# Optimization experiments

Measured on AMD Instinct MI355X. Metric: run time of the kernel, lower is better.

Reference implementation:

```python
import jax, jax.numpy as jnp
import numpy as np

N = 100000   # num_nodes
R = 200      # num_relations
DIM = 200    # hidden dim (in = out for every layer)
B = 30       # num_bases
L = 2        # num_layers
E = 800000   # num_edges


def setup_inputs() -> dict:
    key = jax.random.key(0)
    ks = jax.random.split(key, 7)
    edge_index = jax.random.randint(ks[0], (2, E), 0, N)
    edge_type = jax.random.randint(ks[1], (E,), 0, R)
    s = 1.0 / np.sqrt(DIM)
    emb = jax.random.normal(ks[2], (N, DIM), jnp.float32)
    comp = jax.random.normal(ks[3], (L, R, B), jnp.float32) * (1.0 / np.sqrt(B))
    bases = jax.random.normal(ks[4], (L, B, DIM, DIM), jnp.float32) * s
    root = jax.random.normal(ks[5], (L, DIM, DIM), jnp.float32) * s
    bias = jnp.zeros((L, DIM), jnp.float32)
    return dict(edge_index=edge_index, edge_type=edge_type, emb=emb,
                comp=comp, bases=bases, root=root, bias=bias)


def _rgcn_layer(x, src, dst, etype, comp_l, bases_l, root_l, bias_l):
    # Basis decomposition: W_r = sum_b comp[r, b] * bases[b]
    # msg_e = x[src_e] @ W_{etype_e}  computed as sum over bases (B is small & fixed)
    x_src = x[src]                      # [E, DIM] gather
    c = comp_l[etype]                   # [E, B] per-edge basis coefficients

    def body(acc, bc):
        basis_b, c_b = bc               # [DIM, DIM], [E]
        return acc + c_b[:, None] * (x_src @ basis_b), None

    acc0 = jnp.zeros((x_src.shape[0], root_l.shape[1]), x.dtype)
    msg, _ = jax.lax.scan(body, acc0, (bases_l, jnp.swapaxes(c, 0, 1)))  # [E, DIM]

    # PyG RGCNConv mean aggregation: normalize by in-degree per (dst node, relation)
    comb = dst * R + etype
    deg = jax.ops.segment_sum(jnp.ones((etype.shape[0],), x.dtype), comb,
                              num_segments=N * R)
    norm = 1.0 / jnp.maximum(deg[comb], 1.0)                             # [E]

    agg = jax.ops.segment_sum(msg * norm[:, None], dst, num_segments=N)  # [N, DIM]
    return agg + x @ root_l + bias_l


def reference(edge_index, edge_type, emb, comp, bases, root, bias):
    src, dst = edge_index[0], edge_index[1]
    x = emb
    for l in range(L):
        x = jax.nn.relu(_rgcn_layer(x, src, dst, edge_type,
                                    comp[l], bases[l], root[l], bias[l]))
        # dropout is identity in eval mode (deterministic reference)
    return x
```

## Files before the change

### kernel.cpp

```cpp
#include <hip/hip_runtime.h>
#include <hip/hip_bf16.h>
#include <stdint.h>

#define NN 100000
#define RR 200
#define DD 200
#define BB 30
#define LL 2
#define EE 800000

#define KP 224
#define NP 208
#define XP 224
#define AP 232
#define BPL 200
#define RT 128
#define MSGP 200
#define NSPL 2
#define MAXNC 24
#define NPART 128
#define EPB ((EE + NPART - 1) / NPART)

using bf16x8 = __attribute__((ext_vector_type(8))) short;
using f32x4  = __attribute__((ext_vector_type(4))) float;

#define OFF_NORM   0ull
#define OFF_SORT   3200000ull
#define OFF_CNT    6400000ull
#define OFF_XB     6404096ull
#define OFF_WT     51204096ull
#define OFF_ROOTT  69840896ull
#define OFF_CTL    69934080ull
#define OFF_POS    70065152ull
#define OFF_DSTCNT 73265152ull
#define OFF_DSTST  73665152ull
#define OFF_CUR    74065184ull
#define OFF_BLKH   74465184ull

static __device__ __forceinline__ short f2bf(float v) {
    union { __hip_bfloat16 h; short s; } u;
    u.h = __float2bfloat16(v);
    return u.s;
}

__global__ void kCount(const int* __restrict__ ei, const int* __restrict__ et,
                       unsigned int* __restrict__ deg8, int* __restrict__ dstCnt, int big) {
    int e = blockIdx.x * 256 + threadIdx.x;
    if (e >= EE) return;
    int d = ei[EE + e];
    int t = et[e];
    int comb = d * RR + t;
    atomicAdd(&deg8[comb >> 2], 1u << ((comb & 3) * 8));
    if (big) atomicAdd(&dstCnt[d], 1);
}

__global__ void kScanBlk(const int* __restrict__ dstCnt, int* __restrict__ dstStart,
                         int* __restrict__ blkSum) {
    __shared__ int s[256];
    int t = threadIdx.x, i = blockIdx.x * 256 + t;
    int v = (i < NN) ? dstCnt[i] : 0;
    s[t] = v;
    __syncthreads();
    #pragma unroll
    for (int off = 1; off < 256; off <<= 1) {
        int x = (t >= off) ? s[t - off] : 0;
        __syncthreads();
        s[t] += x;
        __syncthreads();
    }
    if (i < NN) dstStart[i] = s[t] - v;
    if (t == 255) blkSum[blockIdx.x] = s[255];
}
__global__ void kScanTop(int* __restrict__ blkSum, int nblk) {
    __shared__ int s[512];
    int t = threadIdx.x;
    int v = (t < nblk) ? blkSum[t] : 0;
    s[t] = v;
    __syncthreads();
    #pragma unroll
    for (int off = 1; off < 512; off <<= 1) {
        int x = (t >= off) ? s[t - off] : 0;
        __syncthreads();
        s[t] += x;
        __syncthreads();
    }
    if (t < nblk) blkSum[t] = s[t] - v;
}
__global__ void kScanAdd(const int* __restrict__ dstCnt, int* __restrict__ dstStart,
                         const int* __restrict__ blkSum) {
    int i = blockIdx.x * 256 + threadIdx.x;
    if (i >= NN) return;
    int v = dstStart[i] + blkSum[blockIdx.x];
    dstStart[i] = v;
    if (i == NN - 1) dstStart[NN] = v + dstCnt[i];
}

__global__ void kChunk(const int* __restrict__ dstStart, int* __restrict__ bS,
                       int* __restrict__ cesS, int NC, int T) {
    int tid = threadIdx.x;
    if (tid > NC) return;
    int v;
    if (tid == NC) v = NN;
    else if (tid == 0) v = 0;
    else {
        int target = tid * T;
        int lo = 0, hi = NN;
        while (lo < hi) {
            int mid = (lo + hi) >> 1;
            if (dstStart[mid] >= target) hi = mid; else lo = mid + 1;
        }
        v = lo;
    }
    bS[tid] = v;
    cesS[tid] = dstStart[v];
}

__global__ __launch_bounds__(256) void kHist(const int* __restrict__ ei,
        const int* __restrict__ et, const int* __restrict__ bS,
        int* __restrict__ blockHist, int NC) {
    __shared__ int hist[MAXNC * RR];
    __shared__ int bsh[MAXNC + 1];
    int tid = threadIdx.x, b = blockIdx.x;
    int NB = NC * RR;
    if (tid <= NC) bsh[tid] = bS[tid];
    for (int i = tid; i < NB; i += 256) hist[i] = 0;
    __syncthreads();
    int ebeg = b * EPB, eend = min(EE, ebeg + EPB);
    for (int e = ebeg + tid; e < eend; e += 256) {
        int d = ei[EE + e];
        int t = et[e];
        int c = 0;
        for (int j = 1; j < NC; ++j) if (d >= bsh[j]) c = j;
        atomicAdd(&hist[c * RR + t], 1);
    }
    __syncthreads();
    for (int i = tid; i < NB; i += 256)
        blockHist[(size_t)b * NB + i] = hist[i];
}

__global__ __launch_bounds__(128) void kScanP(int* __restrict__ blockHist,
                                              int* __restrict__ cntB, int NB) {
    __shared__ int s[NPART];
    int t = threadIdx.x, k = blockIdx.x;
    int v = blockHist[(size_t)t * NB + k];
    s[t] = v;
    __syncthreads();
    #pragma unroll
    for (int off = 1; off < NPART; off <<= 1) {
        int x = (t >= off) ? s[t - off] : 0;
        __syncthreads();
        s[t] += x;
        __syncthreads();
    }
    blockHist[(size_t)t * NB + k] = s[t] - v;
    if (t == NPART - 1) cntB[k] = s[NPART - 1];
}

__global__ void kScanB(const int* __restrict__ cntB, int* __restrict__ relStartB,
                       int* __restrict__ cursorB, int nb) {
    __shared__ int c[MAXNC * RR];
    __shared__ int rs[MAXNC * RR + 1];
    int tid = threadIdx.x;
    for (int i = tid; i < nb; i += 256) c[i] = cntB[i];
    __syncthreads();
    if (tid == 0) {
        int s = 0;
        for (int i = 0; i < nb; ++i) {
            rs[i] = s;
            s += c[i];
        }
        rs[nb] = s;
    }
    __syncthreads();
    for (int i = tid; i <= nb; i += 256) {
        relStartB[i] = rs[i];
        if (i < nb) cursorB[i] = rs[i];
    }
}

__global__ __launch_bounds__(256) void kPart(const int* __restrict__ ei,
        const int* __restrict__ et, const unsigned int* __restrict__ deg8,
        const int* __restrict__ bS, const int* __restrict__ relStartB,
        const int* __restrict__ blockHist, const int* __restrict__ dstStart,
        int* __restrict__ cur, float* __restrict__ norm, int* __restrict__ sortedE,
        int* __restrict__ posDst, int NC) {
    __shared__ int curL[MAXNC * RR];
    __shared__ int bsh[MAXNC + 1];
    int tid = threadIdx.x, b = blockIdx.x;
    int NB = NC * RR;
    if (tid <= NC) bsh[tid] = bS[tid];
    for (int i = tid; i < NB; i += 256)
        curL[i] = relStartB[i] + blockHist[(size_t)b * NB + i];
    __syncthreads();
    int ebeg = b * EPB, eend = min(EE, ebeg + EPB);
    for (int e = ebeg + tid; e < eend; e += 256) {
        int d = ei[EE + e];
        int t = et[e];
        int comb = d * RR + t;
        unsigned int deg = (deg8[comb >> 2] >> ((comb & 3) * 8)) & 0xffu;
        norm[e] = 1.0f / (float)(deg ? deg : 1u);
        int c = 0;
        for (int j = 1; j < NC; ++j) if (d >= bsh[j]) c = j;
        int pos = atomicAdd(&curL[c * RR + t], 1);
        sortedE[pos] = e;
        posDst[e] = dstStart[d] + atomicAdd(&cur[d], 1);
    }
}

__global__ void kCountB(const int* __restrict__ ei, const int* __restrict__ et,
                        const int* __restrict__ bS, int* __restrict__ cntB, int NC) {
    __shared__ int bsh[MAXNC + 1];
    if (threadIdx.x <= NC) bsh[threadIdx.x] = bS[threadIdx.x];
    __syncthreads();
    int e = blockIdx.x * 256 + threadIdx.x;
    if (e >= EE) return;
    int d = ei[EE + e];
    int t = et[e];
    int c = 0;
    for (int j = 1; j < NC; ++j) if (d >= bsh[j]) c = j;
    atomicAdd(&cntB[c * RR + t], 1);
}

__global__ void kNormScatter(const int* __restrict__ ei, const int* __restrict__ et,
                             const unsigned int* __restrict__ deg8, const int* __restrict__ bS,
                             int* __restrict__ cursorB, const int* __restrict__ dstStart,
                             int* __restrict__ cur, float* __restrict__ norm,
                             int* __restrict__ sortedE, int* __restrict__ posDst,
                             int NC, int big) {
    __shared__ int bsh[MAXNC + 1];
    if (threadIdx.x <= NC) bsh[threadIdx.x] = bS[threadIdx.x];
    __syncthreads();
    int e = blockIdx.x * 256 + threadIdx.x;
    if (e >= EE) return;
    int d = ei[EE + e];
    int t = et[e];
    int comb = d * RR + t;
    unsigned int deg = (deg8[comb >> 2] >> ((comb & 3) * 8)) & 0xffu;
    norm[e] = 1.0f / (float)(deg ? deg : 1u);
    int c = 0;
    for (int j = 1; j < NC; ++j) if (d >= bsh[j]) c = j;
    int pos = atomicAdd(&cursorB[c * RR + t], 1);
    sortedE[pos] = e;
    if (big) posDst[e] = dstStart[d] + atomicAdd(&cur[d], 1);
}

__global__ void kConvert(const float* __restrict__ x, short* __restrict__ xb, int doRelu) {
    int idx = blockIdx.x * 256 + threadIdx.x;
    if (idx >= NN * XP) return;
    int i = idx / XP, col = idx - i * XP;
    float v = 0.0f;
    if (col < DD) {
        v = x[i * DD + col];
        if (doRelu) v = fmaxf(v, 0.0f);
    }
    xb[idx] = (col < DD) ? f2bf(v) : (short)0;
}

__global__ void kRelu(float* __restrict__ y) {
    int idx = blockIdx.x * 256 + threadIdx.x;
    if (idx < NN * DD) y[idx] = fmaxf(y[idx], 0.0f);
}

__global__ __launch_bounds__(256) void kW(const float* __restrict__ comp,
                                          const float* __restrict__ bases,
                                          short* __restrict__ Wt) {
    int kt = blockIdx.x;
    int ng = blockIdx.y;
    int tid = threadIdx.x;
    int k = kt * 32 + (tid & 31);
    int n = ng * 8 + (tid >> 5);
    bool live = (k < DD) && (n < DD);
    float vb[BB];
    #pragma unroll
    for (int b = 0; b < BB; ++b)
        vb[b] = live ? bases[((size_t)b * DD + k) * DD + n] : 0.0f;
    size_t wo = (size_t)n * KP + k;
    for (int r = 0; r < RR; ++r) {
        float a = 0.0f;
        #pragma unroll
        for (int b = 0; b < BB; ++b) a += comp[r * BB + b] * vb[b];
        Wt[(size_t)r * (NP * KP) + wo] = f2bf(a);
    }
}

__global__ void kRootT(const float* __restrict__ root, short* __restrict__ rootT) {
    int idx = blockIdx.x * 256 + threadIdx.x;
    if (idx >= NP * KP) return;
    int n = idx / KP, k = idx - n * KP;
    rootT[idx] = (n < DD && k < DD) ? f2bf(root[k * DD + n]) : (short)0;
}

template<int F0, int NF>
__device__ __forceinline__ void gemmHalf2(const short* As, const short* bCol,
                                          int arow0, int arow1, int kg,
                                          f32x4* acc0, f32x4* acc1) {
    #pragma unroll
    for (int f = 0; f < NF; ++f) {
        acc0[f] = (f32x4){0.f, 0.f, 0.f, 0.f};
        acc1[f] = (f32x4){0.f, 0.f, 0.f, 0.f};
    }
    bf16x8 bb[2][NF];
    #pragma unroll
    for (int f = 0; f < NF; ++f)
        bb[0][f] = *(const bf16x8*)(bCol + (size_t)(F0 + f) * 16 * KP);
    #pragma unroll
    for (int kc = 0; kc < 7; ++kc) {
        if (kc < 6) {
            #pragma unroll
            for (int f = 0; f < NF; ++f)
                bb[(kc + 1) & 1][f] = *(const bf16x8*)(bCol + (size_t)(F0 + f) * 16 * KP + (kc + 1) * 32);
        }
        bf16x8 a0 = *(const bf16x8*)(&As[arow0 * AP + kc * 32 + kg]);
        bf16x8 a1 = *(const bf16x8*)(&As[arow1 * AP + kc * 32 + kg]);
        #pragma unroll
        for (int f = 0; f < NF; ++f) {
            acc0[f] = __builtin_amdgcn_mfma_f32_16x16x32_bf16(a0, bb[kc & 1][f], acc0[f], 0, 0, 0);
            acc1[f] = __builtin_amdgcn_mfma_f32_16x16x32_bf16(a1, bb[kc & 1][f], acc1[f], 0, 0, 0);
        }
    }
}

__global__ __launch_bounds__(256) void kRootGemm(const short* __restrict__ xb,
        const short* __restrict__ rootT, const float* __restrict__ bias,
        float* __restrict__ y) {
    __shared__ short As[RT * AP];
    int i0 = blockIdx.x * RT;
    int tid = threadIdx.x;
    int rowL = tid >> 1, sub = tid & 1;
    int i = i0 + rowL;
    for (int c = sub; c < 28; c += 2) {
        int4 v = make_int4(0, 0, 0, 0);
        if (i < NN) v = *(const int4*)(xb + (size_t)i * XP + c * 8);
        *(int4*)(&As[rowL * AP + c * 8]) = v;
    }
    __syncthreads();
    int lane = tid & 63, wave = tid >> 6;
    int arow0 = wave * 32 + (lane & 15);
    int arow1 = arow0 + 16;
    int kg = (lane >> 4) * 8;
    const short* bCol = rootT + (lane & 15) * KP + kg;
    int colLane = lane & 15;
    int rbase = i0 + wave * 32 + (lane >> 4) * 4;
    {
        f32x4 acc0[7], acc1[7];
        gemmHalf2<0, 7>(As, bCol, arow0, arow1, kg, acc0, acc1);
        #pragma unroll
        for (int f = 0; f < 7; ++f) {
            int col = f * 16 + colLane;
            float bv = bias[col];
            #pragma unroll
            for (int j = 0; j < 4; ++j) {
                int r0 = rbase + j, r1 = rbase + 16 + j;
                if (r0 < NN) y[(size_t)r0 * DD + col] = acc0[f][j] + bv;
                if (r1 < NN) y[(size_t)r1 * DD + col] = acc1[f][j] + bv;
            }
        }
    }
    {
        f32x4 acc0[6], acc1[6];
        gemmHalf2<7, 6>(As, bCol, arow0, arow1, kg, acc0, acc1);
        #pragma unroll
        for (int f = 0; f < 6; ++f) {
            int col = (7 + f) * 16 + colLane;
            if (col < DD) {
                float bv = bias[col];
                #pragma unroll
                for (int j = 0; j < 4; ++j) {
                    int r0 = rbase + j, r1 = rbase + 16 + j;
                    if (r0 < NN) y[(size_t)r0 * DD + col] = acc0[f][j] + bv;
                    if (r1 < NN) y[(size_t)r1 * DD + col] = acc1[f][j] + bv;
                }
            }
        }
    }
}

template<int MODE>
__global__ __launch_bounds__(512) void kMsgP(const int* __restrict__ ei,
        const short* __restrict__ xb, const short* __restrict__ Wt,
        const int* __restrict__ relStartB, const int* __restrict__ sortedE,
        const float* __restrict__ norm, const int* __restrict__ posDst,
        const int* __restrict__ cesS, float* __restrict__ y,
        short* __restrict__ msg, int c) {
    __shared__ short Bp[200 * BPL + 64];
    int r = blockIdx.x / NSPL;
    int h = blockIdx.x - r * NSPL;
    int relStart = relStartB[c * RR + r];
    int eEnd     = relStartB[c * RR + r + 1];
    int nE = eEnd - relStart;
    if (nE <= 0) return;
    int tid = threadIdx.x;
    {
        const short* wp = Wt + (size_t)r * (NP * KP);
        for (int idx = tid; idx < 200 * 25; idx += 512) {
            int n = idx / 25, k8 = idx - n * 25;
            int4 v = *(const int4*)(wp + (size_t)n * KP + k8 * 8);
            *(int4*)(&Bp[n * BPL + k8 * 8]) = v;
        }
    }
    __syncthreads();
    int lane = tid & 63, wave = tid >> 6;
    int colLane = lane & 15;
    int kg = (lane >> 4) * 8;
    int rbase = (lane >> 4) * 4;
    int nwt = (nE + 31) / 32;
    int ces = (MODE == 0) ? cesS[c] : 0;

    bf16x8 aC[2][7], aN[2][7];
    int psC[2][4], psN[2][4];
    float nmC[2][4], nmN[2][4];

    auto loadTile = [&](int wt, bf16x8 (*a)[7], int (*ps)[4], float (*nm)[4]) {
        int eBase = relStart + wt * 32;
        #pragma unroll
        for (int m = 0; m < 2; ++m) {
            int eIdxA = eBase + m * 16 + colLane;
            int eidA = sortedE[min(eIdxA, eEnd - 1)];
            int srcA = ei[eidA];
            const short* aRow = xb + (size_t)srcA * XP;
            #pragma unroll
            for (int kc = 0; kc < 7; ++kc)
                a[m][kc] = *(const bf16x8*)(aRow + kc * 32 + kg);
            #pragma unroll
            for (int j = 0; j < 4; ++j) {
                int eI = eBase + m * 16 + rbase + j;
                bool v = eI < eEnd;
                int eid = v ? sortedE[eI] : 0;
                nm[m][j] = v ? norm[eid] : 0.0f;
                if (MODE == 0) ps[m][j] = v ? (posDst[eid] - ces) : -1;
                else           ps[m][j] = v ? ei[EE + eid] : -1;
            }
        }
    };

    int wt = h * 8 + wave;
    if (wt < nwt) loadTile(wt, aC, psC, nmC);
    for (; wt < nwt; wt += NSPL * 8) {
        int wtn = wt + NSPL * 8;
        if (wtn < nwt) loadTile(wtn, aN, psN, nmN);
        {
            f32x4 acc0[7], acc1[7];
            #pragma unroll
            for (int f = 0; f < 7; ++f) {
                acc0[f] = (f32x4){0.f, 0.f, 0.f, 0.f};
                acc1[f] = (f32x4){0.f, 0.f, 0.f, 0.f};
            }
            #pragma unroll
            for (int kc = 0; kc < 7; ++kc) {
                bf16x8 bb[7];
                #pragma unroll
                for (int f = 0; f < 7; ++f)
                    bb[f] = *(const bf16x8*)(&Bp[(f * 16 + colLane) * BPL + kc * 32 + kg]);
                #pragma unroll
                for (int f = 0; f < 7; ++f) {
                    acc0[f] = __builtin_amdgcn_mfma_f32_16x16x32_bf16(aC[0][kc], bb[f], acc0[f], 0, 0, 0);
                    acc1[f] = __builtin_amdgcn_mfma_f32_16x16x32_bf16(aC[1][kc], bb[f], acc1[f], 0, 0, 0);
                }
            }
            #pragma unroll
            for (int m = 0; m < 2; ++m) {
                #pragma unroll
                for (int j = 0; j < 4; ++j) {
                    int ps = psC[m][j]; float nm = nmC[m][j];
                    if (ps >= 0) {
                        #pragma unroll
                        for (int f = 0; f < 7; ++f) {
                            int col = f * 16 + colLane;
                            float val = (m ? acc1[f][j] : acc0[f][j]) * nm;
                            if (MODE == 0) msg[(size_t)ps * MSGP + col] = f2bf(val);
                            else           atomicAdd(&y[(size_t)ps * DD + col], val);
                        }
                    }
                }
            }
        }
        {
            f32x4 acc0[6], acc1[6];
            #pragma unroll
            for (int f = 0; f < 6; ++f) {
                acc0[f] = (f32x4){0.f, 0.f, 0.f, 0.f};
                acc1[f] = (f32x4){0.f, 0.f, 0.f, 0.f};
            }
            #pragma unroll
            for (int kc = 0; kc < 7; ++kc) {
                bf16x8 bb[6];
                #pragma unroll
                for (int f = 0; f < 6; ++f) {
                    int row = (7 + f) * 16 + colLane;
                    row = min(row, 199);
                    bb[f] = *(const bf16x8*)(&Bp[row * BPL + kc * 32 + kg]);
                }
                #pragma unroll
                for (int f = 0; f < 6; ++f) {
                    acc0[f] = __builtin_amdgcn_mfma_f32_16x16x32_bf16(aC[0][kc], bb[f], acc0[f], 0, 0, 0);
                    acc1[f] = __builtin_amdgcn_mfma_f32_16x16x32_bf16(aC[1][kc], bb[f], acc1[f], 0, 0, 0);
                }
            }
            #pragma unroll
            for (int m = 0; m < 2; ++m) {
                #pragma unroll
                for (int j = 0; j < 4; ++j) {
                    int ps = psC[m][j]; float nm = nmC[m][j];
                    if (ps >= 0) {
                        #pragma unroll
                        for (int f = 0; f < 6; ++f) {
                            int col = (7 + f) * 16 + colLane;
                            if (col < DD) {
                                float val = (m ? acc1[f][j] : acc0[f][j]) * nm;
                                if (MODE == 0) msg[(size_t)ps * MSGP + col] = f2bf(val);
                                else           atomicAdd(&y[(size_t)ps * DD + col], val);
                            }
                        }
                    }
                }
            }
        }
        if (wtn < nwt) {
            #pragma unroll
            for (int m = 0; m < 2; ++m) {
                #pragma unroll
                for (int kc = 0; kc < 7; ++kc) aC[m][kc] = aN[m][kc];
                #pragma unroll
                for (int j = 0; j < 4; ++j) { psC[m][j] = psN[m][j]; nmC[m][j] = nmN[m][j]; }
            }
        }
    }
}

__global__ __launch_bounds__(256) void kAgg(const short* __restrict__ msg,
        const int* __restrict__ dstStart, const int* __restrict__ bS,
        const int* __restrict__ cesS, float* __restrict__ y, int c) {
    int wv = threadIdx.x >> 6, lane = threadIdx.x & 63;
    int b0 = bS[c], b1 = bS[c + 1];
    int ces = cesS[c];
    int gw = blockIdx.x * 4 + wv;
    int nw = gridDim.x * 4;
    for (int d = b0 + gw; d < b1; d += nw) {
        int s = dstStart[d] - ces, e = dstStart[d + 1] - ces;
        float a0 = 0.f, a1 = 0.f, a2 = 0.f, a3 = 0.f;
        if (lane < 50) {
            for (int j = s; j < e; ++j) {
                int2 v = *(const int2*)(msg + (size_t)j * MSGP + lane * 4);
                unsigned u0 = (unsigned)v.x, u1 = (unsigned)v.y;
                a0 += __uint_as_float(u0 << 16);
                a1 += __uint_as_float(u0 & 0xffff0000u);
                a2 += __uint_as_float(u1 << 16);
                a3 += __uint_as_float(u1 & 0xffff0000u);
            }
            int colBase = lane * 4;
            float4 rv = *(const float4*)(y + (size_t)d * DD + colBase);
            float4 o;
            o.x = fmaxf(rv.x + a0, 0.f);
            o.y = fmaxf(rv.y + a1, 0.f);
            o.z = fmaxf(rv.z + a2, 0.f);
            o.w = fmaxf(rv.w + a3, 0.f);
            *(float4*)(y + (size_t)d * DD + colBase) = o;
        }
    }
}

extern "C" void kernel_launch(void* const* d_in, const int* in_sizes, int n_in,
                              void* d_out, int out_size, void* d_ws, size_t ws_size,
                              hipStream_t stream) {
    (void)in_sizes; (void)n_in; (void)out_size;
    const int*   ei    = (const int*)d_in[0];
    const int*   et    = (const int*)d_in[1];
    const float* emb   = (const float*)d_in[2];
    const float* comp  = (const float*)d_in[3];
    const float* bases = (const float*)d_in[4];
    const float* root  = (const float*)d_in[5];
    const float* bias  = (const float*)d_in[6];
    float* y = (float*)d_out;
    char* ws = (char*)d_ws;
    float* norm    = (float*)(ws + OFF_NORM);
    int*   sortedE = (int*)(ws + OFF_SORT);
    short* xb      = (short*)(ws + OFF_XB);
    short* Wt      = (short*)(ws + OFF_WT);
    short* rootT   = (short*)(ws + OFF_ROOTT);
    int*   posDst  = (int*)(ws + OFF_POS);
    int*   dstCnt  = (int*)(ws + OFF_DSTCNT);
    int*   dstStart= (int*)(ws + OFF_DSTST);
    int*   cur     = (int*)(ws + OFF_CUR);
    int*   blockHist = (int*)(ws + OFF_BLKH);
    unsigned int* deg8 = (unsigned int*)(ws + OFF_XB);

    int NC = 0;
    long long T = EE;
    unsigned long long msgOff = 0;
    for (int cc = 1; cc <= MAXNC; ++cc) {
        long long t = (EE + cc - 1) / cc;
        unsigned long long mo = OFF_BLKH + (unsigned long long)NPART * cc * RR * 4;
        unsigned long long need = mo + (unsigned long long)(t + 64) * (MSGP * 2);
        if ((unsigned long long)ws_size >= need) { NC = cc; T = t; msgOff = mo; break; }
    }
    int big = (NC > 0) ? 1 : 0;
    if (!big) { NC = 1; T = EE; msgOff = OFF_BLKH; }
    short* msg = (short*)(ws + msgOff);

    int *cntB, *relStartB, *cursorB, *bS, *cesS, *blkSum;
    if (big) {
        int* ctl = (int*)(ws + OFF_CTL);
        cntB = ctl; relStartB = ctl + 4864; cursorB = ctl + 9728;
        bS = ctl + 19456; cesS = ctl + 19520; blkSum = ctl + 19584;
    } else {
        int* ctl = (int*)(ws + OFF_CNT);
        cntB = ctl; relStartB = ctl + 256; cursorB = ctl + 512;
        bS = ctl + 976; cesS = ctl + 992; blkSum = ctl + 1000;
    }

    const int NBLK = (NN + 255) / 256;

    hipMemsetAsync(deg8, 0, (size_t)NN * RR, stream);
    if (big) {
        hipMemsetAsync(dstCnt, 0, (size_t)NN * 4, stream);
        hipMemsetAsync(cur, 0, (size_t)NN * 4, stream);
    } else {
        hipMemsetAsync((void*)cntB, 0, 4096, stream);
    }

    kCount<<<(EE + 255) / 256, 256, 0, stream>>>(ei, et, deg8, dstCnt, big);
    if (big) {
        kScanBlk<<<NBLK, 256, 0, stream>>>(dstCnt, dstStart, blkSum);
        kScanTop<<<1, 512, 0, stream>>>(blkSum, NBLK);
        kScanAdd<<<NBLK, 256, 0, stream>>>(dstCnt, dstStart, blkSum);
        kChunk<<<1, 64, 0, stream>>>(dstStart, bS, cesS, NC, (int)T);
        kHist<<<NPART, 256, 0, stream>>>(ei, et, bS, blockHist, NC);
        kScanP<<<NC * RR, NPART, 0, stream>>>(blockHist, cntB, NC * RR);
        kScanB<<<1, 256, 0, stream>>>(cntB, relStartB, cursorB, NC * RR);
        kPart<<<NPART, 256, 0, stream>>>(ei, et, deg8, bS, relStartB, blockHist,
                                         dstStart, cur, norm, sortedE, posDst, NC);
    } else {
        kCountB<<<(EE + 255) / 256, 256, 0, stream>>>(ei, et, bS, cntB, NC);
        kScanB<<<1, 256, 0, stream>>>(cntB, relStartB, cursorB, NC * RR);
        kNormScatter<<<(EE + 255) / 256, 256, 0, stream>>>(ei, et, deg8, bS, cursorB,
                                                           dstStart, cur, norm, sortedE,
                                                           posDst, NC, big);
    }
    kConvert<<<(NN * XP + 255) / 256, 256, 0, stream>>>(emb, xb, 0);

    for (int l = 0; l < LL; ++l) {
        kW<<<dim3(7, 26), 256, 0, stream>>>(comp + l * RR * BB,
                                            bases + (size_t)l * BB * DD * DD, Wt);
        kRootT<<<(NP * KP + 255) / 256, 256, 0, stream>>>(root + l * DD * DD, rootT);
        kRootGemm<<<(NN + RT - 1) / RT, 256, 0, stream>>>(xb, rootT, bias + l * DD, y);
        if (big) {
            for (int c = 0; c < NC; ++c) {
                kMsgP<0><<<RR * NSPL, 512, 0, stream>>>(ei, xb, Wt, relStartB, sortedE,
                                                        norm, posDst, cesS, y, msg, c);
                kAgg<<<2048, 256, 0, stream>>>(msg, dstStart, bS, cesS, y, c);
            }
            if (l == 0)
                kConvert<<<(NN * XP + 255) / 256, 256, 0, stream>>>(y, xb, 0);
        } else {
            kMsgP<1><<<RR * NSPL, 512, 0, stream>>>(ei, xb, Wt, relStartB, sortedE,
                                                    norm, posDst, cesS, y, msg, 0);
            if (l == 0) kConvert<<<(NN * XP + 255) / 256, 256, 0, stream>>>(y, xb, 1);
            else        kRelu<<<(NN * DD + 255) / 256, 256, 0, stream>>>(y);
        }
    }
}
```

Before: 1.301 ms.

## Shrink LDS weight tile to 160 rows, stream rest from global, drop prefetch

Only the first 160 output rows of each relation's weight matrix are now staged in LDS; the last 48 rows (columns 160-207) are read straight from global memory with a double-buffered register prefetch over k. The register double-buffering of the next edge tile's A fragments and indices is removed. The goal is to cut LDS use and register pressure so more blocks or waves fit per CU. The cost is extra global/L2 weight reads per tile and no overlap of the gather latency with compute.

```diff
diff --git a/kernel.cpp b/kernel.cpp
--- a/kernel.cpp
+++ b/kernel.cpp
@@ -14,6 +14,7 @@
 #define XP 224
 #define AP 232
 #define BPL 200
+#define LROWS 160
 #define RT 128
 #define MSGP 200
 #define NSPL 2
@@ -382,7 +383,7 @@
         const float* __restrict__ norm, const int* __restrict__ posDst,
         const int* __restrict__ cesS, float* __restrict__ y,
         short* __restrict__ msg, int c) {
-    __shared__ short Bp[200 * BPL + 64];
+    __shared__ short Bp[LROWS * BPL + 64];
     int r = blockIdx.x / NSPL;
     int h = blockIdx.x - r * NSPL;
     int relStart = relStartB[c * RR + r];
@@ -390,13 +391,11 @@
     int nE = eEnd - relStart;
     if (nE <= 0) return;
     int tid = threadIdx.x;
-    {
-        const short* wp = Wt + (size_t)r * (NP * KP);
-        for (int idx = tid; idx < 200 * 25; idx += 512) {
-            int n = idx / 25, k8 = idx - n * 25;
-            int4 v = *(const int4*)(wp + (size_t)n * KP + k8 * 8);
-            *(int4*)(&Bp[n * BPL + k8 * 8]) = v;
-        }
+    const short* wp = Wt + (size_t)r * (NP * KP);
+    for (int idx = tid; idx < LROWS * 25; idx += 512) {
+        int n = idx / 25, k8 = idx - n * 25;
+        int4 v = *(const int4*)(wp + (size_t)n * KP + k8 * 8);
+        *(int4*)(&Bp[n * BPL + k8 * 8]) = v;
     }
     __syncthreads();
     int lane = tid & 63, wave = tid >> 6;
@@ -405,12 +404,13 @@
     int rbase = (lane >> 4) * 4;
     int nwt = (nE + 31) / 32;
     int ces = (MODE == 0) ? cesS[c] : 0;
-
-    bf16x8 aC[2][7], aN[2][7];
-    int psC[2][4], psN[2][4];
-    float nmC[2][4], nmN[2][4];
-
-    auto loadTile = [&](int wt, bf16x8 (*a)[7], int (*ps)[4], float (*nm)[4]) {
+    const short* gCol = wp + (size_t)(LROWS + colLane) * KP + kg;
+
+    bf16x8 aC[2][7];
+    int psC[2][4];
+    float nmC[2][4];
+
+    for (int wt = h * 8 + wave; wt < nwt; wt += NSPL * 8) {
         int eBase = relStart + wt * 32;
         #pragma unroll
         for (int m = 0; m < 2; ++m) {
@@ -420,24 +420,17 @@
             const short* aRow = xb + (size_t)srcA * XP;
             #pragma unroll
             for (int kc = 0; kc < 7; ++kc)
-                a[m][kc] = *(const bf16x8*)(aRow + kc * 32 + kg);
+                aC[m][kc] = *(const bf16x8*)(aRow + kc * 32 + kg);
             #pragma unroll
             for (int j = 0; j < 4; ++j) {
                 int eI = eBase + m * 16 + rbase + j;
                 bool v = eI < eEnd;
                 int eid = v ? sortedE[eI] : 0;
-                nm[m][j] = v ? norm[eid] : 0.0f;
-                if (MODE == 0) ps[m][j] = v ? (posDst[eid] - ces) : -1;
-                else           ps[m][j] = v ? ei[EE + eid] : -1;
-            }
-        }
-    };
-
-    int wt = h * 8 + wave;
-    if (wt < nwt) loadTile(wt, aC, psC, nmC);
-    for (; wt < nwt; wt += NSPL * 8) {
-        int wtn = wt + NSPL * 8;
-        if (wtn < nwt) loadTile(wtn, aN, psN, nmN);
+                nmC[m][j] = v ? norm[eid] : 0.0f;
+                if (MODE == 0) psC[m][j] = v ? (posDst[eid] - ces) : -1;
+                else           psC[m][j] = v ? ei[EE + eid] : -1;
+            }
+        }
         {
             f32x4 acc0[7], acc1[7];
             #pragma unroll
@@ -481,19 +474,27 @@
                 acc0[f] = (f32x4){0.f, 0.f, 0.f, 0.f};
                 acc1[f] = (f32x4){0.f, 0.f, 0.f, 0.f};
             }
+            bf16x8 gg[2][3];
+            #pragma unroll
+            for (int ff = 0; ff < 3; ++ff)
+                gg[0][ff] = *(const bf16x8*)(gCol + (size_t)ff * 16 * KP);
             #pragma unroll
             for (int kc = 0; kc < 7; ++kc) {
-                bf16x8 bb[6];
+                if (kc < 6) {
+                    #pragma unroll
+                    for (int ff = 0; ff < 3; ++ff)
+                        gg[(kc + 1) & 1][ff] = *(const bf16x8*)(gCol + (size_t)ff * 16 * KP + (kc + 1) * 32);
+                }
+                bf16x8 bb[3];
                 #pragma unroll
-                for (int f = 0; f < 6; ++f) {
-                    int row = (7 + f) * 16 + colLane;
-                    row = min(row, 199);
-                    bb[f] = *(const bf16x8*)(&Bp[row * BPL + kc * 32 + kg]);
-                }
+                for (int ff = 0; ff < 3; ++ff)
+                    bb[ff] = *(const bf16x8*)(&Bp[((7 + ff) * 16 + colLane) * BPL + kc * 32 + kg]);
                 #pragma unroll
-                for (int f = 0; f < 6; ++f) {
-                    acc0[f] = __builtin_amdgcn_mfma_f32_16x16x32_bf16(aC[0][kc], bb[f], acc0[f], 0, 0, 0);
-                    acc1[f] = __builtin_amdgcn_mfma_f32_16x16x32_bf16(aC[1][kc], bb[f], acc1[f], 0, 0, 0);
+                for (int ff = 0; ff < 3; ++ff) {
+                    acc0[ff] = __builtin_amdgcn_mfma_f32_16x16x32_bf16(aC[0][kc], bb[ff], acc0[ff], 0, 0, 0);
+                    acc1[ff] = __builtin_amdgcn_mfma_f32_16x16x32_bf16(aC[1][kc], bb[ff], acc1[ff], 0, 0, 0);
+                    acc0[3 + ff] = __builtin_amdgcn_mfma_f32_16x16x32_bf16(aC[0][kc], gg[kc & 1][ff], acc0[3 + ff], 0, 0, 0);
+                    acc1[3 + ff] = __builtin_amdgcn_mfma_f32_16x16x32_bf16(aC[1][kc], gg[kc & 1][ff], acc1[3 + ff], 0, 0, 0);
                 }
             }
             #pragma unroll
@@ -513,15 +514,6 @@
                         }
                     }
                 }
-            }
-        }
-        if (wtn < nwt) {
-            #pragma unroll
-            for (int m = 0; m < 2; ++m) {
-                #pragma unroll
-                for (int kc = 0; kc < 7; ++kc) aC[m][kc] = aN[m][kc];
-                #pragma unroll
-                for (int j = 0; j < 4; ++j) { psC[m][j] = psN[m][j]; nmC[m][j] = nmN[m][j]; }
             }
         }
     }
```

Result: no change. 1.284 ms (-1.4%).
